# Performance work log

Hardware: AMD Instinct MI355X
Metric: run time of the kernel (lower is better)

The kernel has to match this reference:

```python
import jax, jax.numpy as jnp
import numpy as np

B, D, U = 4096, 1024, 1024

def cumax(a):
    # Faithful to source: softmax over last axis, cumsum over axis 0 (TF defaults).
    return jnp.cumsum(jax.nn.softmax(a, axis=-1), axis=0)

def setup_inputs() -> dict:
    key = jax.random.key(0)
    ks = jax.random.split(key, 21)
    names = ['inputs', 'hidden_prev', 'cell_prev',
             'Wf', 'Uf', 'bf', 'Wi', 'Ui', 'bi', 'Wo', 'Uo', 'bo',
             'Wc', 'Uc', 'bc', 'Wft', 'Uft', 'bft', 'Wit', 'Uit', 'bit']
    shapes = [(B, D), (B, U), (B, U)] + [(D, U), (U, U), (U,)] * 6
    scales = [1.0, 1.0, 1.0] + [0.05, 0.05, 0.05] * 6  # random_normal init ~ small stddev
    return {n: jax.random.normal(k, s, dtype=jnp.float32) * sc
            for n, k, s, sc in zip(names, ks, shapes, scales)}

def reference(inputs, hidden_prev, cell_prev,
              Wf, Uf, bf, Wi, Ui, bi, Wo, Uo, bo,
              Wc, Uc, bc, Wft, Uft, bft, Wit, Uit, bit):
    # Fuse the 12 small GEMMs into 2 big ones: [B,D]@[D,6U] and [B,U]@[U,6U]
    W_all = jnp.concatenate([Wf, Wi, Wo, Wc, Wft, Wit], axis=1)   # [D, 6U]
    U_all = jnp.concatenate([Uf, Ui, Uo, Uc, Uft, Uit], axis=1)   # [U, 6U]
    b_all = jnp.concatenate([bf, bi, bo, bc, bft, bit], axis=0)   # [6U]
    pre = inputs @ W_all + hidden_prev @ U_all + b_all            # [B, 6U]
    zf, zi, zo, zc, zft, zit = [pre[:, j*U:(j+1)*U] for j in range(6)]

    f = jax.nn.sigmoid(zf)
    i = jax.nn.sigmoid(zi)
    o = jax.nn.sigmoid(zo)
    c_hat = jnp.tanh(zc)
    f_tilde = cumax(zft)
    i_tilde = 1.0 - cumax(zit)

    omega = f_tilde * i_tilde
    f_hat = f * omega + (f_tilde - omega)
    i_hat = i * omega + (i_tilde - omega)
    cell = f_hat * cell_prev + i_hat * c_hat
    hidden = o * jnp.tanh(cell)
    return hidden, cell
```

## Files before the change

### kernel.cpp

```cpp
#include <hip/hip_runtime.h>
#include <cstdint>
#include <cstddef>


typedef _Float16 half8  __attribute__((ext_vector_type(8)));
typedef _Float16 half4v __attribute__((ext_vector_type(4)));
typedef float f32x4 __attribute__((ext_vector_type(4)));

__device__ __forceinline__ void async16(const _Float16* g, _Float16* l) {
  __builtin_amdgcn_global_load_lds(
      (const __attribute__((address_space(1))) void*)g,
      (__attribute__((address_space(3))) void*)l, 16, 0, 0);
}

struct Ptrs12 { const float* p[12]; };
struct Ptrs6  { const float* p[6];  };

__global__ void prep(const float* __restrict__ X, const float* __restrict__ H,
                     Ptrs12 w, Ptrs6 bs,
                     _Float16* __restrict__ Ahi, _Float16* __restrict__ Bhi,
                     float* __restrict__ b_all) {
  __shared__ float tile[64][65];
  const int blk = blockIdx.x;
  const int t = threadIdx.x;
  if (blk < 8192) {
    size_t base = ((size_t)blk * 256 + t) * 4;
    int k = (int)(base & 2047);
    size_t b = base >> 11;
    const float* src = (k < 1024) ? (X + b * 1024 + k) : (H + b * 1024 + (k - 1024));
    float4 v = *(const float4*)src;
    half4v hi = { (_Float16)v.x, (_Float16)v.y, (_Float16)v.z, (_Float16)v.w };
    *(half4v*)(Ahi + base) = hi;
  } else if (blk < 11264) {
    int bb = blk - 8192;
    int mat = bb >> 8;
    int tl = bb & 255;
    int tr = tl >> 4, tc = tl & 15;
    int g = mat >> 1, s = mat & 1;
    const float* src = w.p[mat];
    int col = t & 63, r0 = t >> 6;
#pragma unroll
    for (int i = 0; i < 16; i++) {
      int row = i * 4 + r0;
      tile[row][col] = src[(size_t)(tr * 64 + row) * 1024 + tc * 64 + col];
    }
    __syncthreads();
    int c2 = t >> 2, kseg = t & 3;
    half8 v0, v1;
#pragma unroll
    for (int j = 0; j < 8; j++) {
      v0[j] = (_Float16)(tile[kseg * 16 + j][c2] * 64.0f);
      v1[j] = (_Float16)(tile[kseg * 16 + 8 + j][c2] * 64.0f);
    }
    size_t n  = (size_t)g * 1024 + tc * 64 + c2;
    size_t kk = (size_t)s * 1024 + tr * 64 + kseg * 16;
    *(half8*)(Bhi + n * 2048 + kk) = v0;
    *(half8*)(Bhi + n * 2048 + kk + 8) = v1;
  } else {
    int n = (blk - 11264) * 256 + t;
    b_all[n] = bs.p[n >> 10][n & 1023];
  }
}

__global__ __launch_bounds__(256) void gemm_split(
    const _Float16* __restrict__ Ah, const _Float16* __restrict__ Bh,
    const float* __restrict__ b_all, _Float16* __restrict__ pre16) {
  __shared__ _Float16 lds[64 * 136];
  _Float16* sAh = lds;
  _Float16* sBh = lds + 4096;

  const int pid = blockIdx.x;
  const int group = pid / (8 * 48);
  const int rem = pid % (8 * 48);
  const int mTile = group * 8 + (rem & 7);
  const int nTile = rem >> 3;

  const int t = threadIdx.x;
  const int lane = t & 63;
  const int wave = t >> 6;
  const int waveM = wave >> 1, waveN = wave & 1;
  const int kgrp = lane >> 4, frow = lane & 15;
  const size_t baseA = (size_t)mTile * 128 * 2048;
  const size_t baseB = (size_t)nTile * 128 * 2048;

  f32x4 acc[4][4] = {};

  for (int ks = 0; ks < 64; ks++) {
    const int k0 = ks * 32;
#pragma unroll
    for (int q = 0; q < 2; q++) {
      int slot = q * 256 + t;
      int r = slot >> 2;
      int sg = slot & 3;
      int sig = sg ^ ((r >> 1) & 3);
      size_t go = (size_t)r * 2048 + k0 + sig * 8;
      async16(Ah + baseA + go, sAh + slot * 8);
      async16(Bh + baseB + go, sBh + slot * 8);
    }
    __syncthreads();

    half8 ah[4], bh[4];
#pragma unroll
    for (int mi = 0; mi < 4; mi++) {
      int r = waveM * 64 + mi * 16 + frow;
      int ps = kgrp ^ ((r >> 1) & 3);
      ah[mi] = *(const half8*)(sAh + r * 32 + ps * 8);
    }
#pragma unroll
    for (int ni = 0; ni < 4; ni++) {
      int r = waveN * 64 + ni * 16 + frow;
      int ps = kgrp ^ ((r >> 1) & 3);
      bh[ni] = *(const half8*)(sBh + r * 32 + ps * 8);
    }
#pragma unroll
    for (int mi = 0; mi < 4; mi++)
#pragma unroll
      for (int ni = 0; ni < 4; ni++)
        acc[mi][ni] = __builtin_amdgcn_mfma_f32_16x16x32_f16(ah[mi], bh[ni], acc[mi][ni], 0, 0, 0);
    __syncthreads();
  }

  const int cbase = nTile * 128;
  float bias[4];
#pragma unroll
  for (int ni = 0; ni < 4; ni++)
    bias[ni] = b_all[cbase + waveN * 64 + ni * 16 + frow];

#pragma unroll
  for (int pass = 0; pass < 2; pass++) {
    if (waveM == pass) {
#pragma unroll
      for (int mi = 0; mi < 4; mi++)
#pragma unroll
        for (int ni = 0; ni < 4; ni++) {
          int colL = waveN * 64 + ni * 16 + frow;
#pragma unroll
          for (int j = 0; j < 4; j++) {
            int rowL = mi * 16 + kgrp * 4 + j;
            lds[rowL * 136 + colL] =
                (_Float16)(acc[mi][ni][j] * (1.0f / 64.0f) + bias[ni]);
          }
        }
    }
    __syncthreads();
#pragma unroll
    for (int rnd = 0; rnd < 4; rnd++) {
      int row = rnd * 16 + (t >> 4);
      int seg = t & 15;
      half8 v = *(const half8*)(lds + row * 136 + seg * 8);
      *(half8*)(pre16 + (size_t)(mTile * 128 + pass * 64 + row) * 6144 + cbase + seg * 8) = v;
    }
    __syncthreads();
  }
}

__global__ void softmax_partials(_Float16* __restrict__ pre16, f32x4* __restrict__ part4) {
  __shared__ float wsum[4][1024];
  int m = blockIdx.x >> 9;
  int ch = blockIdx.x & 511;
  int t = threadIdx.x;
  int wave = t >> 6, lane = t & 63;
  f32x4 colacc[4] = {};
  for (int rr = 0; rr < 2; rr++) {
    int b = ch * 8 + wave * 2 + rr;
    _Float16* row = pre16 + (size_t)b * 6144 + (4 + m) * 1024;
    f32x4 v[4];
    float mx = -3.4e38f;
#pragma unroll
    for (int j = 0; j < 4; j++) {
      half4v h = *(const half4v*)(row + lane * 4 + 256 * j);
      v[j] = f32x4{ (float)h[0], (float)h[1], (float)h[2], (float)h[3] };
      mx = fmaxf(mx, fmaxf(fmaxf(v[j][0], v[j][1]), fmaxf(v[j][2], v[j][3])));
    }
#pragma unroll
    for (int off = 32; off > 0; off >>= 1) mx = fmaxf(mx, __shfl_xor(mx, off, 64));
    float sum = 0.f;
#pragma unroll
    for (int j = 0; j < 4; j++)
#pragma unroll
      for (int q = 0; q < 4; q++) { v[j][q] = __expf(v[j][q] - mx); sum += v[j][q]; }
#pragma unroll
    for (int off = 32; off > 0; off >>= 1) sum += __shfl_xor(sum, off, 64);
    float inv = 1.f / sum;
#pragma unroll
    for (int j = 0; j < 4; j++) {
      v[j] *= inv;
      half4v h = { (_Float16)v[j][0], (_Float16)v[j][1], (_Float16)v[j][2], (_Float16)v[j][3] };
      *(half4v*)(row + lane * 4 + 256 * j) = h;
      colacc[j] += v[j];
    }
  }
#pragma unroll
  for (int j = 0; j < 4; j++)
    *(f32x4*)(&wsum[wave][lane * 4 + 256 * j]) = colacc[j];
  __syncthreads();
  f32x4 s = *(const f32x4*)(&wsum[0][t * 4]);
  s += *(const f32x4*)(&wsum[1][t * 4]);
  s += *(const f32x4*)(&wsum[2][t * 4]);
  s += *(const f32x4*)(&wsum[3][t * 4]);
  part4[((size_t)m * 256 + t) * 512 + ch] = s;
}

__global__ void scan_partials(const f32x4* __restrict__ part4, f32x4* __restrict__ off4) {
  int gidx = blockIdx.x * 4 + (threadIdx.x >> 6);
  int lane = threadIdx.x & 63;
  size_t base = (size_t)gidx * 512;
  f32x4 v[8];
  f32x4 s = {};
#pragma unroll
  for (int j = 0; j < 8; j++) {
    v[j] = part4[base + lane * 8 + j];
    s += v[j];
  }
  f32x4 incl = s;
#pragma unroll
  for (int off = 1; off < 64; off <<= 1) {
    f32x4 o;
#pragma unroll
    for (int q = 0; q < 4; q++) o[q] = __shfl_up(incl[q], off, 64);
    if (lane >= off) incl += o;
  }
  f32x4 run = incl - s;
#pragma unroll
  for (int j = 0; j < 8; j++) {
    off4[base + lane * 8 + j] = run;
    run += v[j];
  }
}

__global__ void onlstm_final(const _Float16* __restrict__ pre16,
                             const float* __restrict__ cprev, const f32x4* __restrict__ off4,
                             float* __restrict__ out) {
  int ch = blockIdx.x;
  int c4 = threadIdx.x;
  int c = c4 * 4;
  f32x4 runf = off4[(size_t)c4 * 512 + ch];
  f32x4 runi = off4[(size_t)(256 + c4) * 512 + ch];
  for (int r = 0; r < 8; r++) {
    int b = ch * 8 + r;
    const _Float16* row = pre16 + (size_t)b * 6144;
    half4v zf = *(const half4v*)(row + c);
    half4v zi = *(const half4v*)(row + 1024 + c);
    half4v zo = *(const half4v*)(row + 2048 + c);
    half4v zc = *(const half4v*)(row + 3072 + c);
    half4v pf = *(const half4v*)(row + 4096 + c);
    half4v pi = *(const half4v*)(row + 5120 + c);
    f32x4 cp = *(const f32x4*)(cprev + (size_t)b * 1024 + c);
    f32x4 hid, cel;
#pragma unroll
    for (int q = 0; q < 4; q++) {
      runf[q] += (float)pf[q];
      runi[q] += (float)pi[q];
      float ft = runf[q], it = 1.f - runi[q];
      float f  = 1.f / (1.f + __expf(-(float)zf[q]));
      float ii = 1.f / (1.f + __expf(-(float)zi[q]));
      float o  = 1.f / (1.f + __expf(-(float)zo[q]));
      float chat = tanhf((float)zc[q]);
      float omega = ft * it;
      float fhat = f * omega + (ft - omega);
      float ihat = ii * omega + (it - omega);
      float cell = fhat * cp[q] + ihat * chat;
      hid[q] = o * tanhf(cell);
      cel[q] = cell;
    }
    *(f32x4*)(out + (size_t)b * 1024 + c) = hid;
    *(f32x4*)(out + (size_t)4194304 + (size_t)b * 1024 + c) = cel;
  }
}

extern "C" void kernel_launch(void* const* d_in, const int* in_sizes, int n_in,
                              void* d_out, int out_size, void* d_ws, size_t ws_size,
                              hipStream_t stream) {
  const float* X = (const float*)d_in[0];
  const float* H = (const float*)d_in[1];
  const float* C = (const float*)d_in[2];

  char* ws = (char*)d_ws;
  _Float16* pre16 = (_Float16*)(ws);
  _Float16* Ahi   = (_Float16*)(ws + 50331648);
  _Float16* Bhi   = (_Float16*)(ws + 67108864);
  float*    b_all = (float*)(ws + 92274688);
  f32x4*    part4 = (f32x4*)(ws + 92299264);
  f32x4*    off4  = (f32x4*)(ws + 96493568);

  Ptrs12 w;
  for (int g = 0; g < 6; g++) {
    w.p[2 * g]     = (const float*)d_in[3 + 3 * g];
    w.p[2 * g + 1] = (const float*)d_in[4 + 3 * g];
  }
  Ptrs6 bs;
  for (int g = 0; g < 6; g++) bs.p[g] = (const float*)d_in[5 + 3 * g];

  prep<<<11288, 256, 0, stream>>>(X, H, w, bs, Ahi, Bhi, b_all);
  gemm_split<<<1536, 256, 0, stream>>>(Ahi, Bhi, b_all, pre16);
  softmax_partials<<<1024, 256, 0, stream>>>(pre16, part4);
  scan_partials<<<128, 256, 0, stream>>>(part4, off4);
  onlstm_final<<<512, 256, 0, stream>>>(pre16, C, off4, (float*)d_out);
}
```

Before: 338.7 us.

## Replace split GEMM with 128x256-tile 8-wave double-buffered phased pipeline

```diff
diff --git a/kernel.cpp b/kernel.cpp
--- a/kernel.cpp
+++ b/kernel.cpp
@@ -62,95 +62,135 @@
   }
 }
 
-__global__ __launch_bounds__(256) void gemm_split(
+
+#define LGKM0 asm volatile("s_waitcnt lgkmcnt(0)" ::: "memory")
+
+__device__ __forceinline__ void wg_barrier() {
+  __builtin_amdgcn_s_barrier();
+  asm volatile("" ::: "memory");
+}
+
+#define PHASE(TT, MH, NH, STAGE_STMT, WAIT_STMT)                               \
+  {                                                                            \
+    const _Float16* bufA_ = lds + ((TT) & 1) * 24576 + (MH) * 4096;            \
+    const _Float16* bufB_ = lds + ((TT) & 1) * 24576 + 8192 + (NH) * 8192;     \
+    half8 af[2][2], bf[2][2];                                                  \
+    _Pragma("unroll")                                                          \
+    for (int f = 0; f < 2; f++) {                                              \
+      int r = wm * 32 + f * 16 + frow;                                         \
+      _Pragma("unroll")                                                        \
+      for (int ks = 0; ks < 2; ks++)                                           \
+        af[f][ks] = *(const half8*)(bufA_ + r * 64 +                           \
+                                    (((ks * 4 + kgrp) ^ (r & 7)) * 8));        \
+    }                                                                          \
+    _Pragma("unroll")                                                          \
+    for (int g = 0; g < 2; g++) {                                              \
+      int r = wn * 32 + g * 16 + frow;                                         \
+      _Pragma("unroll")                                                        \
+      for (int ks = 0; ks < 2; ks++)                                           \
+        bf[g][ks] = *(const half8*)(bufB_ + r * 64 +                           \
+                                    (((ks * 4 + kgrp) ^ (r & 7)) * 8));        \
+    }                                                                          \
+    STAGE_STMT;                                                                \
+    LGKM0;                                                                     \
+    WAIT_STMT;                                                                 \
+    wg_barrier();                                                              \
+    __builtin_amdgcn_s_setprio(1);                                             \
+    _Pragma("unroll")                                                          \
+    for (int f = 0; f < 2; f++)                                                \
+      _Pragma("unroll")                                                        \
+      for (int g = 0; g < 2; g++)                                              \
+        _Pragma("unroll")                                                      \
+        for (int ks = 0; ks < 2; ks++)                                         \
+          acc[(MH) * 2 + f][(NH) * 2 + g] =                                    \
+              __builtin_amdgcn_mfma_f32_16x16x32_f16(                          \
+                  af[f][ks], bf[g][ks], acc[(MH) * 2 + f][(NH) * 2 + g],       \
+                  0, 0, 0);                                                    \
+    __builtin_amdgcn_s_setprio(0);                                             \
+  }
+
+__global__ __launch_bounds__(512, 2) void gemm_8ph(
     const _Float16* __restrict__ Ah, const _Float16* __restrict__ Bh,
     const float* __restrict__ b_all, _Float16* __restrict__ pre16) {
-  __shared__ _Float16 lds[64 * 136];
-  _Float16* sAh = lds;
-  _Float16* sBh = lds + 4096;
-
-  const int pid = blockIdx.x;
-  const int group = pid / (8 * 48);
-  const int rem = pid % (8 * 48);
-  const int mTile = group * 8 + (rem & 7);
-  const int nTile = rem >> 3;
+  __shared__ __attribute__((aligned(16))) _Float16 lds[49152];
+
+  const int bid = blockIdx.x;
+  const int swz = (bid & 7) * 96 + (bid >> 3);
+  const int nTile = swz / 32;
+  const int mTile = swz % 32;
 
   const int t = threadIdx.x;
   const int lane = t & 63;
   const int wave = t >> 6;
-  const int waveM = wave >> 1, waveN = wave & 1;
+  const int wm = wave >> 2, wn = wave & 3;
   const int kgrp = lane >> 4, frow = lane & 15;
-  const size_t baseA = (size_t)mTile * 128 * 2048;
-  const size_t baseB = (size_t)nTile * 128 * 2048;
+
+  const _Float16* Abase = Ah + (size_t)mTile * 128 * 2048;
+  const _Float16* Bbase = Bh + (size_t)nTile * 256 * 2048;
 
   f32x4 acc[4][4] = {};
 
-  for (int ks = 0; ks < 64; ks++) {
-    const int k0 = ks * 32;
+  auto stageA = [&](int kt, int mh) {
+    int r = t >> 3, k8 = t & 7;
+    int xs = k8 ^ (r & 7);
+    const _Float16* g = Abase + (size_t)(mh * 64 + r) * 2048 + kt * 64 + xs * 8;
+    _Float16* l = lds + (kt & 1) * 24576 + mh * 4096 + t * 8;
+    async16(g, l);
+  };
+  auto stageB = [&](int kt, int nh) {
 #pragma unroll
     for (int q = 0; q < 2; q++) {
-      int slot = q * 256 + t;
-      int r = slot >> 2;
-      int sg = slot & 3;
-      int sig = sg ^ ((r >> 1) & 3);
-      size_t go = (size_t)r * 2048 + k0 + sig * 8;
-      async16(Ah + baseA + go, sAh + slot * 8);
-      async16(Bh + baseB + go, sBh + slot * 8);
-    }
-    __syncthreads();
-
-    half8 ah[4], bh[4];
-#pragma unroll
-    for (int mi = 0; mi < 4; mi++) {
-      int r = waveM * 64 + mi * 16 + frow;
-      int ps = kgrp ^ ((r >> 1) & 3);
-      ah[mi] = *(const half8*)(sAh + r * 32 + ps * 8);
-    }
-#pragma unroll
-    for (int ni = 0; ni < 4; ni++) {
-      int r = waveN * 64 + ni * 16 + frow;
-      int ps = kgrp ^ ((r >> 1) & 3);
-      bh[ni] = *(const half8*)(sBh + r * 32 + ps * 8);
-    }
-#pragma unroll
-    for (int mi = 0; mi < 4; mi++)
-#pragma unroll
-      for (int ni = 0; ni < 4; ni++)
-        acc[mi][ni] = __builtin_amdgcn_mfma_f32_16x16x32_f16(ah[mi], bh[ni], acc[mi][ni], 0, 0, 0);
-    __syncthreads();
-  }
-
-  const int cbase = nTile * 128;
+      int s = q * 512 + t;
+      int r = s >> 3, k8 = s & 7;
+      int xs = k8 ^ (r & 7);
+      const _Float16* g = Bbase + (size_t)(nh * 128 + r) * 2048 + kt * 64 + xs * 8;
+      _Float16* l = lds + (kt & 1) * 24576 + 8192 + nh * 8192 + s * 8;
+      async16(g, l);
+    }
+  };
+
+  stageA(0, 0); stageB(0, 0); stageA(0, 1); stageB(0, 1);
+  stageA(1, 0); stageB(1, 0);
+  asm volatile("s_waitcnt vmcnt(3)" ::: "memory");
+  wg_barrier();
+
+#pragma unroll 2
+  for (int T = 0; T < 32; T++) {
+    PHASE(T, 0, 0, { if (T + 1 < 32) stageA(T + 1, 1); }, {});
+    PHASE(T, 0, 1, { if (T + 1 < 32) stageB(T + 1, 1); }, {});
+    PHASE(T, 1, 0, { if (T + 2 < 32) stageA(T + 2, 0); }, {});
+    PHASE(T, 1, 1, { if (T + 2 < 32) stageB(T + 2, 0); },
+          { if (T < 30) { asm volatile("s_waitcnt vmcnt(3)" ::: "memory"); }
+            else        { asm volatile("s_waitcnt vmcnt(0)" ::: "memory"); } });
+  }
+
+  const float inv64 = 1.0f / 64.0f;
+  const int cb = nTile * 256;
   float bias[4];
 #pragma unroll
-  for (int ni = 0; ni < 4; ni++)
-    bias[ni] = b_all[cbase + waveN * 64 + ni * 16 + frow];
-
-#pragma unroll
-  for (int pass = 0; pass < 2; pass++) {
-    if (waveM == pass) {
-#pragma unroll
-      for (int mi = 0; mi < 4; mi++)
-#pragma unroll
-        for (int ni = 0; ni < 4; ni++) {
-          int colL = waveN * 64 + ni * 16 + frow;
-#pragma unroll
-          for (int j = 0; j < 4; j++) {
-            int rowL = mi * 16 + kgrp * 4 + j;
-            lds[rowL * 136 + colL] =
-                (_Float16)(acc[mi][ni][j] * (1.0f / 64.0f) + bias[ni]);
-          }
-        }
-    }
-    __syncthreads();
-#pragma unroll
-    for (int rnd = 0; rnd < 4; rnd++) {
-      int row = rnd * 16 + (t >> 4);
-      int seg = t & 15;
-      half8 v = *(const half8*)(lds + row * 136 + seg * 8);
-      *(half8*)(pre16 + (size_t)(mTile * 128 + pass * 64 + row) * 6144 + cbase + seg * 8) = v;
-    }
-    __syncthreads();
+  for (int nj = 0; nj < 4; nj++) {
+    int col = (nj >> 1) * 128 + wn * 32 + (nj & 1) * 16 + frow;
+    bias[nj] = b_all[cb + col];
+  }
+#pragma unroll
+  for (int mi = 0; mi < 4; mi++) {
+#pragma unroll
+    for (int nj = 0; nj < 4; nj++) {
+      int row = (mi >> 1) * 64 + wm * 32 + (mi & 1) * 16 + kgrp * 4;
+      int col = (nj >> 1) * 128 + wn * 32 + (nj & 1) * 16 + frow;
+#pragma unroll
+      for (int j = 0; j < 4; j++)
+        lds[(row + j) * 264 + col] =
+            (_Float16)(acc[mi][nj][j] * inv64 + bias[nj]);
+    }
+  }
+  __syncthreads();
+#pragma unroll
+  for (int rr = 0; rr < 8; rr++) {
+    int L = rr * 4096 + t * 8;
+    int row = L >> 8, col = L & 255;
+    half8 v = *(const half8*)(lds + row * 264 + col);
+    *(half8*)(pre16 + (size_t)(mTile * 128 + row) * 6144 + cb + col) = v;
   }
 }
 
@@ -292,7 +332,7 @@
   for (int g = 0; g < 6; g++) bs.p[g] = (const float*)d_in[5 + 3 * g];
 
   prep<<<11288, 256, 0, stream>>>(X, H, w, bs, Ahi, Bhi, b_all);
-  gemm_split<<<1536, 256, 0, stream>>>(Ahi, Bhi, b_all, pre16);
+  gemm_8ph<<<768, 512, 0, stream>>>(Ahi, Bhi, b_all, pre16);
   softmax_partials<<<1024, 256, 0, stream>>>(pre16, part4);
   scan_partials<<<128, 256, 0, stream>>>(part4, off4);
   onlstm_final<<<512, 256, 0, stream>>>(pre16, C, off4, (float*)d_out);
```

Result: faster. 329.8 us (-2.6%).
